# Performance work log

Measured on AMD Instinct MI355X. Metric: run time of the kernel, lower is better.

## Reference

```python
import jax, jax.numpy as jnp
import numpy as np

L, H, E, HS, T, B, V = 6, 12, 768, 64, 1024, 2, 32000
EPS = 1e-5


def layer_norm(x, g, b):
    mu = jnp.mean(x, axis=-1, keepdims=True)
    var = jnp.mean(jnp.square(x - mu), axis=-1, keepdims=True)
    return (x - mu) * jax.lax.rsqrt(var + EPS) * g + b


def setup_inputs() -> dict:
    key = jax.random.key(0)
    ks = jax.random.split(key, 24)
    s = 0.02
    inp = {
        "idx": jax.random.randint(ks[0], (B, T), 0, V),
        "targets": jax.random.randint(ks[1], (B, T), 0, V),
        "tok_emb": jax.random.normal(ks[2], (V, E), jnp.float32) * s,
        "pos_emb": jax.random.normal(ks[3], (T, E), jnp.float32) * s,
        "ln1_g": jnp.ones((L, E), jnp.float32),
        "ln1_b": jnp.zeros((L, E), jnp.float32),
        "wq": jax.random.normal(ks[4], (L, E, E), jnp.float32) * s,
        "wk": jax.random.normal(ks[5], (L, E, E), jnp.float32) * s,
        "wv": jax.random.normal(ks[6], (L, E, E), jnp.float32) * s,
        "wproj": jax.random.normal(ks[7], (L, E, E), jnp.float32) * s,
        "bproj": jnp.zeros((L, E), jnp.float32),
        "ln2_g": jnp.ones((L, E), jnp.float32),
        "ln2_b": jnp.zeros((L, E), jnp.float32),
        "w1": jax.random.normal(ks[8], (L, E, 4 * E), jnp.float32) * s,
        "b1": jnp.zeros((L, 4 * E), jnp.float32),
        "w2": jax.random.normal(ks[9], (L, 4 * E, E), jnp.float32) * s,
        "b2": jnp.zeros((L, E), jnp.float32),
        "lnf_g": jnp.ones((E,), jnp.float32),
        "lnf_b": jnp.zeros((E,), jnp.float32),
        "lm_w": jax.random.normal(ks[10], (E, V), jnp.float32) * s,
        "lm_b": jnp.zeros((V,), jnp.float32),
    }
    return inp


def reference(idx, targets, tok_emb, pos_emb, ln1_g, ln1_b, wq, wk, wv, wproj,
              bproj, ln2_g, ln2_b, w1, b1, w2, b2, lnf_g, lnf_b, lm_w, lm_b):
    x = tok_emb[idx] + pos_emb[None, :T, :]  # [B,T,E]
    causal = jnp.tril(jnp.ones((T, T), bool))
    scale = E ** (-0.5)  # NOTE: original scales by n_embed**-0.5, not head_size
    for l in range(L):
        h = layer_norm(x, ln1_g[l], ln1_b[l])
        q = (h @ wq[l]).reshape(B, T, H, HS)
        k = (h @ wk[l]).reshape(B, T, H, HS)
        v = (h @ wv[l]).reshape(B, T, H, HS)
        scores = jnp.einsum('bqhd,bkhd->bhqk', q, k) * scale
        scores = jnp.where(causal[None, None], scores, -jnp.inf)
        w = jax.nn.softmax(scores, axis=-1)
        attn = jnp.einsum('bhqk,bkhd->bqhd', w, v).reshape(B, T, E)
        # original MultiHeadAttention applies proj TWICE (faithful reproduction)
        out = attn @ wproj[l] + bproj[l]
        out = out @ wproj[l] + bproj[l]
        x = x + out
        h2 = layer_norm(x, ln2_g[l], ln2_b[l])
        x = x + (jax.nn.relu(h2 @ w1[l] + b1[l]) @ w2[l] + b2[l])
    x = layer_norm(x, lnf_g, lnf_b)
    logits = x @ lm_w + lm_b  # [B,T,V]
    logp = jax.nn.log_softmax(logits, axis=-1)
    nll = -jnp.take_along_axis(logp, targets[..., None], axis=-1)[..., 0]
    loss = jnp.mean(nll)
    return logits, loss
```

## Files before the change

kernel.cpp:

```cpp
#include <hip/hip_runtime.h>
#include <math.h>

#define NL 6
#define NH 12
#define NE 768
#define NHS 64
#define NT 1024
#define NB 2
#define NV 32000
#define NM (NB * NT)
#define NQKV (3 * NE)
#define NFF (4 * NE)
#define LN_EPS 1e-5f

typedef __attribute__((ext_vector_type(8))) short short8;
typedef __attribute__((ext_vector_type(4))) float f32x4;
typedef __attribute__((ext_vector_type(4))) unsigned short ushort4v;
typedef __attribute__((address_space(1))) const unsigned int as1_cuint;
typedef __attribute__((address_space(3))) unsigned int as3_uint;

__device__ __forceinline__ unsigned short f2bf(float f) {
    unsigned int u = __builtin_bit_cast(unsigned int, f);
    u += 0x7fffu + ((u >> 16) & 1u);
    return (unsigned short)(u >> 16);
}
__device__ __forceinline__ float bf2f(unsigned short u) {
    unsigned int v = ((unsigned int)u) << 16;
    return __builtin_bit_cast(float, v);
}
__device__ __forceinline__ void gload_lds16(const void* g, void* l) {
    __builtin_amdgcn_global_load_lds((as1_cuint*)g, (as3_uint*)l, 16, 0, 0);
}

__global__ __launch_bounds__(256) void embed_ln_kernel(const int* __restrict__ idx,
                                                       const float* __restrict__ tok,
                                                       const float* __restrict__ pos,
                                                       const float* __restrict__ g,
                                                       const float* __restrict__ b,
                                                       float* __restrict__ x,
                                                       unsigned short* __restrict__ hbuf) {
    __shared__ float red[256];
    int row = blockIdx.x, tid = threadIdx.x;
    int t = row % NT;
    int id = idx[row];
    float v[3]; float s = 0.f;
    #pragma unroll
    for (int k = 0; k < 3; ++k) {
        int c = tid + k * 256;
        v[k] = tok[(long)id * NE + c] + pos[(long)t * NE + c];
        x[(long)row * NE + c] = v[k];
        s += v[k];
    }
    red[tid] = s; __syncthreads();
    for (int o = 128; o > 0; o >>= 1) { if (tid < o) red[tid] += red[tid + o]; __syncthreads(); }
    float mu = red[0] / NE;
    __syncthreads();
    float vr = 0.f;
    #pragma unroll
    for (int k = 0; k < 3; ++k) { float d = v[k] - mu; vr += d * d; }
    red[tid] = vr; __syncthreads();
    for (int o = 128; o > 0; o >>= 1) { if (tid < o) red[tid] += red[tid + o]; __syncthreads(); }
    float rstd = rsqrtf(red[0] / NE + LN_EPS);
    #pragma unroll
    for (int k = 0; k < 3; ++k) {
        int c = tid + k * 256;
        hbuf[(long)row * NE + c] = f2bf((v[k] - mu) * rstd * g[c] + b[c]);
    }
}

template<int S>
__global__ __launch_bounds__(256) void combine_ln_kernel(const float* __restrict__ parts,
                                                         const float* __restrict__ bias,
                                                         float* __restrict__ x,
                                                         const float* __restrict__ g,
                                                         const float* __restrict__ b,
                                                         unsigned short* __restrict__ hbuf) {
    __shared__ float red[256];
    int row = blockIdx.x, tid = threadIdx.x;
    float v[3]; float s = 0.f;
    #pragma unroll
    for (int k = 0; k < 3; ++k) {
        int c = tid + k * 256;
        long i = (long)row * NE + c;
        float a = parts[i];
        #pragma unroll
        for (int si = 1; si < S; ++si) a += parts[(long)si * NM * NE + i];
        a += bias[c] + x[i];
        x[i] = a;
        v[k] = a; s += a;
    }
    red[tid] = s; __syncthreads();
    for (int o = 128; o > 0; o >>= 1) { if (tid < o) red[tid] += red[tid + o]; __syncthreads(); }
    float mu = red[0] / NE;
    __syncthreads();
    float vr = 0.f;
    #pragma unroll
    for (int k = 0; k < 3; ++k) { float d = v[k] - mu; vr += d * d; }
    red[tid] = vr; __syncthreads();
    for (int o = 128; o > 0; o >>= 1) { if (tid < o) red[tid] += red[tid + o]; __syncthreads(); }
    float rstd = rsqrtf(red[0] / NE + LN_EPS);
    #pragma unroll
    for (int k = 0; k < 3; ++k) {
        int c = tid + k * 256;
        hbuf[(long)row * NE + c] = f2bf((v[k] - mu) * rstd * g[c] + b[c]);
    }
}

__global__ __launch_bounds__(256) void transpose4b_kernel(const float* __restrict__ wq,
                                                          const float* __restrict__ wk,
                                                          const float* __restrict__ wv,
                                                          const float* __restrict__ wp,
                                                          unsigned short* __restrict__ wqkvT,
                                                          unsigned short* __restrict__ wprojT) {
    __shared__ float t[32][33];
    int z = blockIdx.z, l = z >> 2, which = z & 3;
    const float* W = ((which == 0) ? wq : (which == 1) ? wk : (which == 2) ? wv : wp) + (long)l * NE * NE;
    unsigned short* WT = (which < 3) ? (wqkvT + (long)l * NQKV * NE + (long)which * NE * NE)
                                     : (wprojT + (long)l * NE * NE);
    int k0 = blockIdx.y * 32, n0 = blockIdx.x * 32;
    int c = threadIdx.x & 31, r = threadIdx.x >> 5;
    #pragma unroll
    for (int p = 0; p < 4; ++p)
        t[r + p * 8][c] = W[(long)(k0 + r + p * 8) * NE + n0 + c];
    __syncthreads();
    #pragma unroll
    for (int p = 0; p < 4; ++p)
        WT[(long)(n0 + r + p * 8) * NE + k0 + c] = f2bf(t[c][r + p * 8]);
}

__global__ __launch_bounds__(256) void transpose_cast_b_kernel(const float* __restrict__ W0,
                                                               unsigned short* __restrict__ WT0,
                                                               int K, int N) {
    __shared__ float t[32][33];
    long lofs = (long)blockIdx.z * K * N;
    const float* W = W0 + lofs;
    unsigned short* WT = WT0 + lofs;
    int k0 = blockIdx.y * 32, n0 = blockIdx.x * 32;
    int c = threadIdx.x & 31, r = threadIdx.x >> 5;
    #pragma unroll
    for (int p = 0; p < 4; ++p)
        t[r + p * 8][c] = W[(long)(k0 + r + p * 8) * N + n0 + c];
    __syncthreads();
    #pragma unroll
    for (int p = 0; p < 4; ++p)
        WT[(long)(n0 + r + p * 8) * K + k0 + c] = f2bf(t[c][r + p * 8]);
}

__global__ __launch_bounds__(256) void cast_kernel(const float* __restrict__ W,
                                                   unsigned short* __restrict__ O, long n) {
    long i = ((long)blockIdx.x * 256 + threadIdx.x) * 4;
    if (i < n) {
        float4 v = *(const float4*)(W + i);
        ushort4v o;
        o[0] = f2bf(v.x); o[1] = f2bf(v.y); o[2] = f2bf(v.z); o[3] = f2bf(v.w);
        *(ushort4v*)(O + i) = o;
    }
}

__global__ __launch_bounds__(256) void beff_b_kernel(const float* __restrict__ bproj,
                                                     const unsigned short* __restrict__ wprojT,
                                                     float* __restrict__ beff) {
    __shared__ float red[256];
    int n = blockIdx.x, l = blockIdx.y, tid = threadIdx.x;
    const unsigned short* wp = wprojT + (long)l * NE * NE + (long)n * NE;
    const float* bp = bproj + (long)l * NE;
    float acc = 0.f;
    for (int j = tid; j < NE; j += 256) acc += bp[j] * bf2f(wp[j]);
    red[tid] = acc; __syncthreads();
    for (int o = 128; o > 0; o >>= 1) { if (tid < o) red[tid] += red[tid + o]; __syncthreads(); }
    if (tid == 0) beff[(long)l * NE + n] = red[0] + bp[n];
}

template<int S>
__global__ __launch_bounds__(256) void combine_kernel(const float* __restrict__ parts,
                                                      unsigned short* __restrict__ bout,
                                                      long total) {
    long i = ((long)blockIdx.x * 256 + threadIdx.x) * 4;
    if (i >= total) return;
    float4 a = *(const float4*)(parts + i);
    #pragma unroll
    for (int s = 1; s < S; ++s) {
        float4 b = *(const float4*)(parts + (long)s * total + i);
        a.x += b.x; a.y += b.y; a.z += b.z; a.w += b.w;
    }
    ushort4v o;
    o[0] = f2bf(a.x); o[1] = f2bf(a.y); o[2] = f2bf(a.z); o[3] = f2bf(a.w);
    *(ushort4v*)(bout + i) = o;
}

template<typename OutT, bool BIAS, bool RELU, int SPLITK>
__global__ __launch_bounds__(256) void gemm_mfma(const unsigned short* __restrict__ A,
                                                 const unsigned short* __restrict__ BT,
                                                 const float* __restrict__ bias,
                                                 OutT* __restrict__ C,
                                                 int gridM, int N, int K) {
    __shared__ unsigned short As[2][128 * 32];
    __shared__ unsigned short Bs[2][128 * 32];
    int tid = threadIdx.x;
    int lane = tid & 63, w = tid >> 6;
    int wr = w >> 1, wc = w & 1;
    int l4 = lane >> 4, l15 = lane & 15;

    int nwg = gridDim.x, orig = blockIdx.x;
    int q = nwg >> 3, r8 = nwg & 7;
    int xcd = orig & 7, ii = orig >> 3;
    int wg = (xcd < r8) ? (xcd * (q + 1) + ii) : (r8 * (q + 1) + (xcd - r8) * q + ii);
    int bm = wg % gridM, bn = wg / gridM;
    int m0 = bm * 128, n0 = bn * 128;

    int kb = K / SPLITK;
    int koff = (SPLITK > 1) ? blockIdx.y * kb : 0;

    f32x4 acc[4][4] = {};

    int srow = lane >> 2;
    int scol = ((lane & 3) ^ ((lane >> 3) & 3)) * 8;
    int rsw  = (l4 ^ ((l15 >> 1) & 3)) * 8;

    #pragma unroll
    for (int it = 0; it < 2; ++it) {
        int rr = w * 32 + it * 16;
        gload_lds16(&A [(long)(m0 + rr + srow) * K + koff + scol], &As[0][rr * 32]);
        gload_lds16(&BT[(long)(n0 + rr + srow) * K + koff + scol], &Bs[0][rr * 32]);
    }

    int cur = 0;
    for (int k0 = 0; k0 < kb; k0 += 32) {
        __syncthreads();
        if (k0 + 32 < kb) {
            #pragma unroll
            for (int it = 0; it < 2; ++it) {
                int rr = w * 32 + it * 16;
                gload_lds16(&A [(long)(m0 + rr + srow) * K + koff + k0 + 32 + scol], &As[cur ^ 1][rr * 32]);
                gload_lds16(&BT[(long)(n0 + rr + srow) * K + koff + k0 + 32 + scol], &Bs[cur ^ 1][rr * 32]);
            }
        }

        short8 a[4], b[4];
        #pragma unroll
        for (int f = 0; f < 4; ++f) {
            a[f] = *(const short8*)&As[cur][(wr * 64 + f * 16 + l15) * 32 + rsw];
            b[f] = *(const short8*)&Bs[cur][(wc * 64 + f * 16 + l15) * 32 + rsw];
        }
        __builtin_amdgcn_s_setprio(1);
        #pragma unroll
        for (int fm = 0; fm < 4; ++fm)
            #pragma unroll
            for (int fn = 0; fn < 4; ++fn)
                acc[fm][fn] = __builtin_amdgcn_mfma_f32_16x16x32_bf16(a[fm], b[fn], acc[fm][fn], 0, 0, 0);
        __builtin_amdgcn_s_setprio(0);
        cur ^= 1;
    }

    if constexpr (SPLITK > 1) {
        float* Cp = (float*)C + (long)blockIdx.y * gridM * 128 * N;
        #pragma unroll
        for (int fm = 0; fm < 4; ++fm)
            #pragma unroll
            for (int j = 0; j < 4; ++j) {
                long row = m0 + wr * 64 + fm * 16 + l4 * 4 + j;
                #pragma unroll
                for (int fn = 0; fn < 4; ++fn)
                    Cp[row * N + n0 + wc * 64 + fn * 16 + l15] = acc[fm][fn][j];
            }
    } else {
        float bs[4];
        #pragma unroll
        for (int fn = 0; fn < 4; ++fn)
            bs[fn] = BIAS ? bias[n0 + wc * 64 + fn * 16 + l15] : 0.f;

        #pragma unroll
        for (int fm = 0; fm < 4; ++fm) {
            #pragma unroll
            for (int j = 0; j < 4; ++j) {
                long row = m0 + wr * 64 + fm * 16 + l4 * 4 + j;
                #pragma unroll
                for (int fn = 0; fn < 4; ++fn) {
                    int col = n0 + wc * 64 + fn * 16 + l15;
                    float v = acc[fm][fn][j] + bs[fn];
                    if (RELU) v = fmaxf(v, 0.f);
                    if constexpr (sizeof(OutT) == 2) C[row * N + col] = (OutT)f2bf(v);
                    else                             C[row * N + col] = v;
                }
            }
        }
    }
}

__global__ __launch_bounds__(256) void gemm_weff_kernel(const unsigned short* __restrict__ A0,
                                                        const unsigned short* __restrict__ B0,
                                                        unsigned short* __restrict__ C0,
                                                        int gridM, int N, int K) {
    __shared__ unsigned short As[2][128 * 32];
    __shared__ unsigned short Bs[2][128 * 32];
    long zofs = (long)blockIdx.z * N * K;
    const unsigned short* A = A0 + zofs;
    const unsigned short* BT = B0 + zofs;
    unsigned short* C = C0 + zofs;
    int tid = threadIdx.x;
    int lane = tid & 63, w = tid >> 6;
    int wr = w >> 1, wc = w & 1;
    int l4 = lane >> 4, l15 = lane & 15;
    int bm = blockIdx.x % gridM, bn = blockIdx.x / gridM;
    int m0 = bm * 128, n0 = bn * 128;

    f32x4 acc[4][4] = {};
    int srow = lane >> 2;
    int scol = ((lane & 3) ^ ((lane >> 3) & 3)) * 8;
    int rsw  = (l4 ^ ((l15 >> 1) & 3)) * 8;

    #pragma unroll
    for (int it = 0; it < 2; ++it) {
        int rr = w * 32 + it * 16;
        gload_lds16(&A [(long)(m0 + rr + srow) * K + scol], &As[0][rr * 32]);
        gload_lds16(&BT[(long)(n0 + rr + srow) * K + scol], &Bs[0][rr * 32]);
    }
    int cur = 0;
    for (int k0 = 0; k0 < K; k0 += 32) {
        __syncthreads();
        if (k0 + 32 < K) {
            #pragma unroll
            for (int it = 0; it < 2; ++it) {
                int rr = w * 32 + it * 16;
                gload_lds16(&A [(long)(m0 + rr + srow) * K + k0 + 32 + scol], &As[cur ^ 1][rr * 32]);
                gload_lds16(&BT[(long)(n0 + rr + srow) * K + k0 + 32 + scol], &Bs[cur ^ 1][rr * 32]);
            }
        }
        short8 a[4], b[4];
        #pragma unroll
        for (int f = 0; f < 4; ++f) {
            a[f] = *(const short8*)&As[cur][(wr * 64 + f * 16 + l15) * 32 + rsw];
            b[f] = *(const short8*)&Bs[cur][(wc * 64 + f * 16 + l15) * 32 + rsw];
        }
        #pragma unroll
        for (int fm = 0; fm < 4; ++fm)
            #pragma unroll
            for (int fn = 0; fn < 4; ++fn)
                acc[fm][fn] = __builtin_amdgcn_mfma_f32_16x16x32_bf16(a[fm], b[fn], acc[fm][fn], 0, 0, 0);
        cur ^= 1;
    }
    #pragma unroll
    for (int fm = 0; fm < 4; ++fm)
        #pragma unroll
        for (int j = 0; j < 4; ++j) {
            long row = m0 + wr * 64 + fm * 16 + l4 * 4 + j;
            #pragma unroll
            for (int fn = 0; fn < 4; ++fn)
                C[row * N + n0 + wc * 64 + fn * 16 + l15] = f2bf(acc[fm][fn][j]);
        }
}

__global__ __launch_bounds__(512, 4) void gemm256x128_lse(const unsigned short* __restrict__ A,
                                                          const unsigned short* __restrict__ BT,
                                                          const float* __restrict__ bias,
                                                          float* __restrict__ C,
                                                          float* __restrict__ pm, float* __restrict__ ps,
                                                          int gridM, int N, int K) {
    __shared__ unsigned short Al[2][256 * 32];
    __shared__ unsigned short Bl[2][128 * 32];
    int tid = threadIdx.x;
    int lane = tid & 63, w = tid >> 6;
    int wm = w >> 1, wn = w & 1;
    int l4 = lane >> 4, l15 = lane & 15;

    int nwg = gridDim.x, orig = blockIdx.x;
    int q = nwg >> 3, r8 = nwg & 7;
    int xcd = orig & 7, ii = orig >> 3;
    int wg = (xcd < r8) ? (xcd * (q + 1) + ii) : (r8 * (q + 1) + (xcd - r8) * q + ii);
    int bm = wg % gridM, bn = wg / gridM;
    int m0 = bm * 256, n0 = bn * 128;

    int nkt = K >> 5;
    int srow = lane >> 2;
    int sslot = ((lane & 3) ^ ((lane >> 3) & 3)) * 8;

    auto STAGE = [&](int slot, int kt) {
        #pragma unroll
        for (int p = 0; p < 2; ++p) {
            int r0 = p * 128 + w * 16;
            gload_lds16(&A[(long)(m0 + r0 + srow) * K + kt * 32 + sslot], &Al[slot][r0 * 32]);
        }
        int r0 = w * 16;
        gload_lds16(&BT[(long)(n0 + r0 + srow) * K + kt * 32 + sslot], &Bl[slot][r0 * 32]);
    };

    f32x4 acc[4][4] = {};
    int rsw = (l4 ^ ((l15 >> 1) & 3)) * 8;

    STAGE(0, 0);
    for (int t = 0; t < nkt; ++t) {
        if (t + 1 < nkt) {
            STAGE((t + 1) & 1, t + 1);
            asm volatile("s_waitcnt vmcnt(3)" ::: "memory");
        } else {
            asm volatile("s_waitcnt vmcnt(0)" ::: "memory");
        }
        asm volatile("s_barrier" ::: "memory");

        int s = t & 1;
        short8 af[4], bf[4];
        #pragma unroll
        for (int f = 0; f < 4; ++f) {
            af[f] = *(const short8*)&Al[s][(wm * 64 + f * 16 + l15) * 32 + rsw];
            bf[f] = *(const short8*)&Bl[s][(wn * 64 + f * 16 + l15) * 32 + rsw];
        }
        asm volatile("s_waitcnt lgkmcnt(0)" ::: "memory");
        asm volatile("s_barrier" ::: "memory");

        __builtin_amdgcn_s_setprio(1);
        #pragma unroll
        for (int fm = 0; fm < 4; ++fm)
            #pragma unroll
            for (int fn = 0; fn < 4; ++fn)
                acc[fm][fn] = __builtin_amdgcn_mfma_f32_16x16x32_bf16(af[fm], bf[fn], acc[fm][fn], 0, 0, 0);
        __builtin_amdgcn_s_setprio(0);
    }

    float bs[4];
    #pragma unroll
    for (int fn = 0; fn < 4; ++fn)
        bs[fn] = bias[n0 + wn * 64 + fn * 16 + l15];

    #pragma unroll
    for (int fm = 0; fm < 4; ++fm) {
        #pragma unroll
        for (int j = 0; j < 4; ++j) {
            long row = m0 + wm * 64 + fm * 16 + l4 * 4 + j;
            float v4[4];
            #pragma unroll
            for (int fn = 0; fn < 4; ++fn) {
                int col = n0 + wn * 64 + fn * 16 + l15;
                float v = acc[fm][fn][j] + bs[fn];
                C[row * N + col] = v;
                v4[fn] = v;
            }
            float mx = fmaxf(fmaxf(v4[0], v4[1]), fmaxf(v4[2], v4[3]));
            #pragma unroll
            for (int off = 1; off < 16; off <<= 1) mx = fmaxf(mx, __shfl_xor(mx, off));
            float sm = 0.f;
            #pragma unroll
            for (int fn = 0; fn < 4; ++fn) sm += __expf(v4[fn] - mx);
            #pragma unroll
            for (int off = 1; off < 16; off <<= 1) sm += __shfl_xor(sm, off);
            if (l15 == 0) {
                int pidx = bn * 2 + wn;
                pm[row * 512 + pidx] = mx;
                ps[row * 512 + pidx] = sm;
            }
        }
    }
}

__global__ __launch_bounds__(256) void vtrans_kernel(const unsigned short* __restrict__ qkv,
                                                     unsigned short* __restrict__ vt) {
    __shared__ unsigned short t[64][72];
    int t0 = blockIdx.x * 64;
    int bh = blockIdx.y;
    int b = bh / NH, h = bh % NH;
    int tid = threadIdx.x;
    #pragma unroll
    for (int i = 0; i < 2; ++i) {
        int r = (tid >> 3) + i * 32, c8 = (tid & 7) * 8;
        short8 v = *(const short8*)(qkv + ((long)b * NT + t0 + r) * NQKV + 2 * NE + h * NHS + c8);
        *(short8*)&t[r][c8] = v;
    }
    __syncthreads();
    #pragma unroll
    for (int i = 0; i < 2; ++i) {
        int d = (tid >> 3) + i * 32, s = (tid & 7) * 8;
        short8 o;
        #pragma unroll
        for (int j = 0; j < 8; ++j) o[j] = (short)t[s + j][d];
        *(short8*)(vt + ((long)bh * NHS + d) * NT + t0 + s) = o;
    }
}

__global__ __launch_bounds__(256) void fattn_kernel(const unsigned short* __restrict__ qkv,
                                                    const unsigned short* __restrict__ vt,
                                                    unsigned short* __restrict__ out) {
    __shared__ unsigned short Ks[2][64 * 64];
    __shared__ unsigned short Vl[2][64 * 64];
    __shared__ unsigned short Ps[4 * 16 * 64];
    int qt = gridDim.x - 1 - blockIdx.x;
    int bh = blockIdx.y;
    int b = bh / NH, h = bh % NH;
    int tid = threadIdx.x, lane = tid & 63, w = tid >> 6;
    int l4 = lane >> 4, l15 = lane & 15;
    long rowb = (long)b * NT;
    const float scale = 0.03608439182435161f;
    const unsigned short* vtp = vt + (long)bh * NHS * NT;

    const unsigned short* qptr = qkv + (rowb + qt * 64 + w * 16 + l15) * NQKV + h * NHS;
    short8 qa0 = *(const short8*)(qptr + l4 * 8);
    short8 qa1 = *(const short8*)(qptr + 32 + l4 * 8);

    f32x4 o[4] = {};
    float m[4], lsum[4];
    #pragma unroll
    for (int j = 0; j < 4; ++j) { m[j] = -INFINITY; lsum[j] = 0.f; }

    int kr_r = tid >> 3, kr_c = (tid & 7) * 8;
    int vr_d = tid >> 3, vr_s = tid & 7;

    short8 kr[2], vr[2];
    auto LOADT = [&](int t) {
        int kbase = t * 64;
        #pragma unroll
        for (int i = 0; i < 2; ++i) {
            kr[i] = *(const short8*)(qkv + (rowb + kbase + kr_r + i * 32) * NQKV + NE + h * NHS + kr_c);
            vr[i] = *(const short8*)(vtp + (long)(vr_d + i * 32) * NT + kbase + vr_s * 8);
        }
    };

    LOADT(0);
    for (int t = 0; t <= qt; ++t) {
        int cur = t & 1;
        #pragma unroll
        for (int i = 0; i < 2; ++i) {
            int r = kr_r + i * 32;
            *(short8*)&Ks[cur][r * 64 + (kr_c ^ ((r & 7) << 3))] = kr[i];
            int d = vr_d + i * 32;
            *(short8*)&Vl[cur][d * 64 + ((vr_s * 8) ^ ((d & 7) << 3))] = vr[i];
        }
        asm volatile("s_waitcnt lgkmcnt(0)" ::: "memory");
        if (t < qt) LOADT(t + 1);
        asm volatile("s_barrier" ::: "memory");

        f32x4 s[4];
        __builtin_amdgcn_s_setprio(1);
        #pragma unroll
        for (int fn = 0; fn < 4; ++fn) {
            int key = fn * 16 + l15;
            short8 kb0 = *(const short8*)&Ks[cur][key * 64 + ((l4 * 8) ^ ((key & 7) << 3))];
            short8 kb1 = *(const short8*)&Ks[cur][key * 64 + ((32 + l4 * 8) ^ ((key & 7) << 3))];
            f32x4 z = {};
            z = __builtin_amdgcn_mfma_f32_16x16x32_bf16(qa0, kb0, z, 0, 0, 0);
            s[fn] = __builtin_amdgcn_mfma_f32_16x16x32_bf16(qa1, kb1, z, 0, 0, 0);
        }
        __builtin_amdgcn_s_setprio(0);

        if (t == qt) {
            #pragma unroll
            for (int fn = 0; fn < 4; ++fn) {
                int key = t * 64 + fn * 16 + l15;
                #pragma unroll
                for (int j = 0; j < 4; ++j) {
                    int qrow = qt * 64 + w * 16 + l4 * 4 + j;
                    s[fn][j] = (key <= qrow) ? s[fn][j] * scale : -1e30f;
                }
            }
        } else {
            #pragma unroll
            for (int fn = 0; fn < 4; ++fn)
                #pragma unroll
                for (int j = 0; j < 4; ++j)
                    s[fn][j] *= scale;
        }

        #pragma unroll
        for (int j = 0; j < 4; ++j) {
            float mj = fmaxf(fmaxf(s[0][j], s[1][j]), fmaxf(s[2][j], s[3][j]));
            #pragma unroll
            for (int off = 1; off < 16; off <<= 1) mj = fmaxf(mj, __shfl_xor(mj, off));
            float mnew = fmaxf(m[j], mj);
            float alpha = __expf(m[j] - mnew);
            m[j] = mnew;
            float psum = 0.f;
            #pragma unroll
            for (int fn = 0; fn < 4; ++fn) {
                float p = __expf(s[fn][j] - mnew);
                psum += p;
                int rr = l4 * 4 + j, c = fn * 16 + l15;
                Ps[w * 1024 + rr * 64 + (c ^ ((rr & 7) << 3))] = f2bf(p);
            }
            #pragma unroll
            for (int off = 1; off < 16; off <<= 1) psum += __shfl_xor(psum, off);
            lsum[j] = lsum[j] * alpha + psum;
            #pragma unroll
            for (int fn = 0; fn < 4; ++fn) o[fn][j] *= alpha;
        }

        short8 pa0 = *(const short8*)&Ps[w * 1024 + l15 * 64 + ((l4 * 8) ^ ((l15 & 7) << 3))];
        short8 pa1 = *(const short8*)&Ps[w * 1024 + l15 * 64 + ((32 + l4 * 8) ^ ((l15 & 7) << 3))];
        __builtin_amdgcn_s_setprio(1);
        #pragma unroll
        for (int fn = 0; fn < 4; ++fn) {
            int d = fn * 16 + l15;
            short8 vb0 = *(const short8*)&Vl[cur][d * 64 + ((l4 * 8) ^ ((d & 7) << 3))];
            short8 vb1 = *(const short8*)&Vl[cur][d * 64 + ((32 + l4 * 8) ^ ((d & 7) << 3))];
            o[fn] = __builtin_amdgcn_mfma_f32_16x16x32_bf16(pa0, vb0, o[fn], 0, 0, 0);
            o[fn] = __builtin_amdgcn_mfma_f32_16x16x32_bf16(pa1, vb1, o[fn], 0, 0, 0);
        }
        __builtin_amdgcn_s_setprio(0);
    }

    #pragma unroll
    for (int j = 0; j < 4; ++j) {
        long row = rowb + qt * 64 + w * 16 + l4 * 4 + j;
        float inv = 1.0f / lsum[j];
        #pragma unroll
        for (int fn = 0; fn < 4; ++fn)
            out[row * NE + h * NHS + fn * 16 + l15] = f2bf(o[fn][j] * inv);
    }
}

__global__ __launch_bounds__(256) void nll_combine_kernel(const float* __restrict__ logits,
                                                          const float* __restrict__ pm,
                                                          const float* __restrict__ ps,
                                                          const int* __restrict__ targets,
                                                          float* __restrict__ nll) {
    __shared__ float rm[256], rs[256];
    int row = blockIdx.x, tid = threadIdx.x;
    float m = -1e30f, s = 0.f;
    for (int i = tid; i < 500; i += 256) {
        float m2 = pm[(long)row * 512 + i], s2 = ps[(long)row * 512 + i];
        float mm = fmaxf(m, m2);
        s = s * __expf(m - mm) + s2 * __expf(m2 - mm);
        m = mm;
    }
    rm[tid] = m; rs[tid] = s; __syncthreads();
    for (int o = 128; o > 0; o >>= 1) {
        if (tid < o) {
            float m2 = rm[tid + o], s2 = rs[tid + o];
            float mm = fmaxf(rm[tid], m2);
            rs[tid] = rs[tid] * __expf(rm[tid] - mm) + s2 * __expf(m2 - mm);
            rm[tid] = mm;
        }
        __syncthreads();
    }
    if (tid == 0) {
        int tgt = targets[row];
        nll[row] = -(logits[(long)row * NV + tgt] - rm[0] - logf(rs[0]));
    }
}

__global__ void loss_reduce_kernel(const float* __restrict__ nll, float* __restrict__ out) {
    __shared__ float red[256];
    int tid = threadIdx.x;
    float s = 0.f;
    for (int i = tid; i < NM; i += 256) s += nll[i];
    red[tid] = s; __syncthreads();
    for (int o = 128; o > 0; o >>= 1) { if (tid < o) red[tid] += red[tid + o]; __syncthreads(); }
    if (tid == 0) out[0] = red[0] / NM;
}

extern "C" void kernel_launch(void* const* d_in, const int* in_sizes, int n_in,
                              void* d_out, int out_size, void* d_ws, size_t ws_size,
                              hipStream_t stream) {
    const int*   idx     = (const int*)  d_in[0];
    const int*   targets = (const int*)  d_in[1];
    const float* tok     = (const float*)d_in[2];
    const float* pos     = (const float*)d_in[3];
    const float* ln1_g   = (const float*)d_in[4];
    const float* ln1_b   = (const float*)d_in[5];
    const float* wq      = (const float*)d_in[6];
    const float* wk      = (const float*)d_in[7];
    const float* wv      = (const float*)d_in[8];
    const float* wproj   = (const float*)d_in[9];
    const float* bproj   = (const float*)d_in[10];
    const float* ln2_g   = (const float*)d_in[11];
    const float* ln2_b   = (const float*)d_in[12];
    const float* w1      = (const float*)d_in[13];
    const float* b1      = (const float*)d_in[14];
    const float* w2      = (const float*)d_in[15];
    const float* b2      = (const float*)d_in[16];
    const float* lnf_g   = (const float*)d_in[17];
    const float* lnf_b   = (const float*)d_in[18];
    const float* lm_w    = (const float*)d_in[19];
    const float* lm_b    = (const float*)d_in[20];

    float* logits = (float*)d_out;
    float* loss   = logits + (long)NM * NV;

    char* p = (char*)d_ws;
    float*          x      = (float*)p;          p += (long)NM * NE * 4;
    unsigned short* hbuf   = (unsigned short*)p; p += (long)NM * NE * 2;
    unsigned short* qkv    = (unsigned short*)p; p += (long)NM * NQKV * 2;
    unsigned short* att    = (unsigned short*)p; p += (long)NM * NE * 2;
    unsigned short* hid    = (unsigned short*)p; p += (long)NM * NFF * 2;
    unsigned short* vt     = (unsigned short*)p; p += (long)NB * NH * NHS * NT * 2;
    float*          nll    = (float*)p;          p += (long)NM * 4;
    float*          pmb    = (float*)p;          p += (long)NM * 512 * 4;
    float*          psb    = (float*)p;          p += (long)NM * 512 * 4;
    float*          parts  = (float*)p;          p += (long)2 * NM * NQKV * 4;
    unsigned short* wqkvT6 = (unsigned short*)p; p += (long)NL * NQKV * NE * 2;
    unsigned short* wprojT6= (unsigned short*)p; p += (long)NL * NE * NE * 2;
    unsigned short* wprojC6= (unsigned short*)p; p += (long)NL * NE * NE * 2;
    unsigned short* weffT6 = (unsigned short*)p; p += (long)NL * NE * NE * 2;
    float*          beff6  = (float*)p;          p += (long)NL * NE * 4;
    unsigned short* w1T6   = (unsigned short*)p; p += (long)NL * NFF * NE * 2;
    unsigned short* w2T6   = (unsigned short*)p; p += (long)NL * NE * NFF * 2;
    unsigned short* lmT    = (unsigned short*)p; p += (long)NV * NE * 2;

    dim3 blk(256);

    transpose4b_kernel<<<dim3(NE / 32, NE / 32, 4 * NL), blk, 0, stream>>>(
        wq, wk, wv, wproj, wqkvT6, wprojT6);
    cast_kernel<<<(NL * NE * NE) / 1024, blk, 0, stream>>>(wproj, wprojC6, (long)NL * NE * NE);
    transpose_cast_b_kernel<<<dim3(NFF / 32, NE / 32, NL), blk, 0, stream>>>(w1, w1T6, NE, NFF);
    transpose_cast_b_kernel<<<dim3(NE / 32, NFF / 32, NL), blk, 0, stream>>>(w2, w2T6, NFF, NE);
    gemm_weff_kernel<<<dim3(36, 1, NL), blk, 0, stream>>>(wprojT6, wprojC6, weffT6, 6, NE, NE);
    beff_b_kernel<<<dim3(NE, NL), blk, 0, stream>>>(bproj, wprojT6, beff6);
    transpose_cast_b_kernel<<<dim3(NV / 32, NE / 32, 1), blk, 0, stream>>>(lm_w, lmT, NE, NV);

    embed_ln_kernel<<<NM, blk, 0, stream>>>(idx, tok, pos, ln1_g, ln1_b, x, hbuf);

    for (int l = 0; l < NL; ++l) {
        gemm_mfma<float, false, false, 2><<<dim3((NM/128)*(NQKV/128), 2), blk, 0, stream>>>(
            hbuf, wqkvT6 + (long)l * NQKV * NE, nullptr, parts, NM / 128, NQKV, NE);
        combine_kernel<2><<<(NM * NQKV) / 1024, blk, 0, stream>>>(parts, qkv, (long)NM * NQKV);
        vtrans_kernel<<<dim3(NT / 64, NB * NH), blk, 0, stream>>>(qkv, vt);
        fattn_kernel<<<dim3(NT / 64, NB * NH), blk, 0, stream>>>(qkv, vt, att);
        gemm_mfma<float, false, false, 2><<<dim3((NM/128)*(NE/128), 2), blk, 0, stream>>>(
            att, weffT6 + (long)l * NE * NE, nullptr, parts, NM / 128, NE, NE);
        combine_ln_kernel<2><<<NM, blk, 0, stream>>>(
            parts, beff6 + (long)l * NE, x, ln2_g + (long)l * NE, ln2_b + (long)l * NE, hbuf);
        gemm_mfma<unsigned short, true, true, 1><<<dim3((NM/128)*(NFF/128)), blk, 0, stream>>>(
            hbuf, w1T6 + (long)l * NFF * NE, b1 + (long)l * NFF, hid, NM / 128, NFF, NE);
        gemm_mfma<float, false, false, 4><<<dim3((NM/128)*(NE/128), 4), blk, 0, stream>>>(
            hid, w2T6 + (long)l * NE * NFF, nullptr, parts, NM / 128, NE, NFF);
        const float* ng = (l < NL - 1) ? (ln1_g + (long)(l + 1) * NE) : lnf_g;
        const float* nb = (l < NL - 1) ? (ln1_b + (long)(l + 1) * NE) : lnf_b;
        combine_ln_kernel<4><<<NM, blk, 0, stream>>>(parts, b2 + (long)l * NE, x, ng, nb, hbuf);
    }

    gemm256x128_lse<<<dim3((NM/256)*(NV/128)), dim3(512), 0, stream>>>(
        hbuf, lmT, lm_b, logits, pmb, psb, NM / 256, NV, NE);
    nll_combine_kernel<<<NM, blk, 0, stream>>>(logits, pmb, psb, targets, nll);
    loss_reduce_kernel<<<1, blk, 0, stream>>>(nll, loss);
}
```

Baseline: 1.180 ms.

## Triple-buffer LDS staging in GEMM kernels and use nontemporal logits stores

Both the generic MFMA GEMM and the LM-head GEMM with fused LSE move from double to triple LDS buffering, so global-to-LDS loads are issued two k-tiles ahead. Explicit vmcnt waits and barriers replace __syncthreads. The intent is to hide more global memory latency behind MFMA work. The large fp32 logits store becomes nontemporal to reduce cache pollution. The cost is 50% more LDS per block, which may lower occupancy (the LSE kernel asks for 4 blocks per CU at 512 threads), and the hand-counted vmcnt values must match the number of loads issued per stage.

```diff
diff --git a/kernel.cpp b/kernel.cpp
--- a/kernel.cpp
+++ b/kernel.cpp
@@ -194,8 +194,8 @@
                                                  const float* __restrict__ bias,
                                                  OutT* __restrict__ C,
                                                  int gridM, int N, int K) {
-    __shared__ unsigned short As[2][128 * 32];
-    __shared__ unsigned short Bs[2][128 * 32];
+    __shared__ unsigned short As[3][128 * 32];
+    __shared__ unsigned short Bs[3][128 * 32];
     int tid = threadIdx.x;
     int lane = tid & 63, w = tid >> 6;
     int wr = w >> 1, wc = w & 1;
@@ -210,6 +210,7 @@
 
     int kb = K / SPLITK;
     int koff = (SPLITK > 1) ? blockIdx.y * kb : 0;
+    int nkt = kb >> 5;
 
     f32x4 acc[4][4] = {};
 
@@ -217,31 +218,36 @@
     int scol = ((lane & 3) ^ ((lane >> 3) & 3)) * 8;
     int rsw  = (l4 ^ ((l15 >> 1) & 3)) * 8;
 
-    #pragma unroll
-    for (int it = 0; it < 2; ++it) {
-        int rr = w * 32 + it * 16;
-        gload_lds16(&A [(long)(m0 + rr + srow) * K + koff + scol], &As[0][rr * 32]);
-        gload_lds16(&BT[(long)(n0 + rr + srow) * K + koff + scol], &Bs[0][rr * 32]);
-    }
-
-    int cur = 0;
-    for (int k0 = 0; k0 < kb; k0 += 32) {
-        __syncthreads();
-        if (k0 + 32 < kb) {
-            #pragma unroll
-            for (int it = 0; it < 2; ++it) {
-                int rr = w * 32 + it * 16;
-                gload_lds16(&A [(long)(m0 + rr + srow) * K + koff + k0 + 32 + scol], &As[cur ^ 1][rr * 32]);
-                gload_lds16(&BT[(long)(n0 + rr + srow) * K + koff + k0 + 32 + scol], &Bs[cur ^ 1][rr * 32]);
-            }
-        }
+    auto STAGE = [&](int slot, int kt) {
+        #pragma unroll
+        for (int it = 0; it < 2; ++it) {
+            int rr = w * 32 + it * 16;
+            gload_lds16(&A [(long)(m0 + rr + srow) * K + koff + kt * 32 + scol], &As[slot][rr * 32]);
+            gload_lds16(&BT[(long)(n0 + rr + srow) * K + koff + kt * 32 + scol], &Bs[slot][rr * 32]);
+        }
+    };
+
+    STAGE(0, 0);
+    if (nkt > 1) STAGE(1, 1);
+
+    int s = 0;
+    for (int t = 0; t < nkt; ++t) {
+        if (t + 2 < nkt) STAGE((t + 2) % 3, t + 2);
+        int ahead = nkt - 1 - t;
+        if (ahead >= 2)      asm volatile("s_waitcnt vmcnt(8)" ::: "memory");
+        else if (ahead == 1) asm volatile("s_waitcnt vmcnt(4)" ::: "memory");
+        else                 asm volatile("s_waitcnt vmcnt(0)" ::: "memory");
+        asm volatile("s_barrier" ::: "memory");
 
         short8 a[4], b[4];
         #pragma unroll
         for (int f = 0; f < 4; ++f) {
-            a[f] = *(const short8*)&As[cur][(wr * 64 + f * 16 + l15) * 32 + rsw];
-            b[f] = *(const short8*)&Bs[cur][(wc * 64 + f * 16 + l15) * 32 + rsw];
-        }
+            a[f] = *(const short8*)&As[s][(wr * 64 + f * 16 + l15) * 32 + rsw];
+            b[f] = *(const short8*)&Bs[s][(wc * 64 + f * 16 + l15) * 32 + rsw];
+        }
+        asm volatile("s_waitcnt lgkmcnt(0)" ::: "memory");
+        asm volatile("s_barrier" ::: "memory");
+
         __builtin_amdgcn_s_setprio(1);
         #pragma unroll
         for (int fm = 0; fm < 4; ++fm)
@@ -249,7 +255,7 @@
             for (int fn = 0; fn < 4; ++fn)
                 acc[fm][fn] = __builtin_amdgcn_mfma_f32_16x16x32_bf16(a[fm], b[fn], acc[fm][fn], 0, 0, 0);
         __builtin_amdgcn_s_setprio(0);
-        cur ^= 1;
+        s = (s + 1) % 3;
     }
 
     if constexpr (SPLITK > 1) {
@@ -356,8 +362,8 @@
                                                           float* __restrict__ C,
                                                           float* __restrict__ pm, float* __restrict__ ps,
                                                           int gridM, int N, int K) {
-    __shared__ unsigned short Al[2][256 * 32];
-    __shared__ unsigned short Bl[2][128 * 32];
+    __shared__ unsigned short Al[3][256 * 32];
+    __shared__ unsigned short Bl[3][128 * 32];
     int tid = threadIdx.x;
     int lane = tid & 63, w = tid >> 6;
     int wm = w >> 1, wn = w & 1;
@@ -388,16 +394,16 @@
     int rsw = (l4 ^ ((l15 >> 1) & 3)) * 8;
 
     STAGE(0, 0);
+    STAGE(1, 1);
+    int s = 0;
     for (int t = 0; t < nkt; ++t) {
-        if (t + 1 < nkt) {
-            STAGE((t + 1) & 1, t + 1);
-            asm volatile("s_waitcnt vmcnt(3)" ::: "memory");
-        } else {
-            asm volatile("s_waitcnt vmcnt(0)" ::: "memory");
-        }
+        if (t + 2 < nkt) STAGE((t + 2) % 3, t + 2);
+        int ahead = nkt - 1 - t;
+        if (ahead >= 2)      asm volatile("s_waitcnt vmcnt(6)" ::: "memory");
+        else if (ahead == 1) asm volatile("s_waitcnt vmcnt(3)" ::: "memory");
+        else                 asm volatile("s_waitcnt vmcnt(0)" ::: "memory");
         asm volatile("s_barrier" ::: "memory");
 
-        int s = t & 1;
         short8 af[4], bf[4];
         #pragma unroll
         for (int f = 0; f < 4; ++f) {
@@ -414,6 +420,7 @@
             for (int fn = 0; fn < 4; ++fn)
                 acc[fm][fn] = __builtin_amdgcn_mfma_f32_16x16x32_bf16(af[fm], bf[fn], acc[fm][fn], 0, 0, 0);
         __builtin_amdgcn_s_setprio(0);
+        s = (s + 1) % 3;
     }
 
     float bs[4];
@@ -431,7 +438,7 @@
             for (int fn = 0; fn < 4; ++fn) {
                 int col = n0 + wn * 64 + fn * 16 + l15;
                 float v = acc[fm][fn][j] + bs[fn];
-                C[row * N + col] = v;
+                __builtin_nontemporal_store(v, &C[row * N + col]);
                 v4[fn] = v;
             }
             float mx = fmaxf(fmaxf(v4[0], v4[1]), fmaxf(v4[2], v4[3]));
```

Result: faster. 1.140 ms (-3.4%).
